# Optimization experiments

Measured on AMD Instinct MI355X. Metric: run time of the kernel, lower is better.

The kernel has to match this reference:

```python
import jax, jax.numpy as jnp
import numpy as np

TEMPERATURE = 0.1
BATCH_SIZE = 4096
NUM_CLASSES = 100
EPS = 1e-10
COS_EPS = 1e-8  # F.cosine_similarity default eps


def setup_inputs() -> dict:
    key = jax.random.key(0)
    k1, k2 = jax.random.split(key)
    pred = jax.random.normal(k1, (4096, 1024), dtype=jnp.float32)
    target = jax.random.randint(k2, (4096,), 0, NUM_CLASSES, dtype=jnp.int64)
    return {"pred": pred, "target": target}


def reference(pred, target):
    n, d = pred.shape
    # cosine similarity via normalize-once + Gram GEMM (same math as pairwise
    # F.cosine_similarity with its eps clamp on the norms)
    norms = jnp.linalg.norm(pred, axis=1, keepdims=True)  # [n,1]
    xn = pred / jnp.maximum(norms, COS_EPS)
    p_norm = xn @ xn.T                                    # [n,n]
    p_norm = jnp.maximum(p_norm, EPS)                     # p_norm[p_norm<eps]=eps
    dist = jnp.exp(p_norm / TEMPERATURE)

    same = target[:, None] == target[None, :]             # [n,n] bool
    eye = jnp.eye(n, dtype=dist.dtype)
    positives = same.astype(dist.dtype) - eye
    negatives = (~same).astype(dist.dtype)

    denominators = jnp.sum(dist * negatives, axis=0)      # [n]
    denominators = jnp.maximum(denominators, EPS)
    numerators = dist * positives
    frac = numerators / denominators[None, :]             # broadcast over rows

    # original does boolean indexing frac[frac>=eps]; equivalent masked log-sum
    valid = frac >= EPS
    safe = jnp.where(valid, frac, 1.0)
    loss = -jnp.sum(jnp.where(valid, jnp.log(safe), 0.0)) / BATCH_SIZE
    return loss
```

## Files before the change

kernel.cpp:

```cpp
#include <hip/hip_runtime.h>
#include <hip/hip_bf16.h>

#define NROWS 4096
#define DIM   1024
#define BT    256
#define BH    128
#define BK    128
#define NKT   (DIM / BK)
#define NTB   (NROWS / BT)
#define NOFF  240
#define TEMP_INV 10.0f
#define INV_S 3.814697e-6f

typedef int i32x4 __attribute__((ext_vector_type(4)));

__device__ __forceinline__ void gload16(const void* g, void* l) {
    __builtin_amdgcn_global_load_lds(
        (const __attribute__((address_space(1))) void*)g,
        (__attribute__((address_space(3))) void*)l, 16, 0, 0);
}

__global__ __launch_bounds__(256) void normalize_k(const float* __restrict__ pred,
                                                   unsigned char* __restrict__ xn,
                                                   float* __restrict__ posw,
                                                   float* __restrict__ denw) {
    const int row = blockIdx.x;
    const int tid = threadIdx.x;
    const float4 v = reinterpret_cast<const float4*>(pred + (size_t)row * DIM)[tid];
    float ss = v.x * v.x + v.y * v.y + v.z * v.z + v.w * v.w;
    #pragma unroll
    for (int off = 32; off; off >>= 1) ss += __shfl_xor(ss, off, 64);
    __shared__ float red[4];
    if ((tid & 63) == 0) red[tid >> 6] = ss;
    __syncthreads();
    const float tot = red[0] + red[1] + red[2] + red[3];
    const float scale = 512.0f / fmaxf(sqrtf(tot), 1e-8f);
    int q0 = __float2int_rn(v.x * scale);
    int q1 = __float2int_rn(v.y * scale);
    int q2 = __float2int_rn(v.z * scale);
    int q3 = __float2int_rn(v.w * scale);
    q0 = min(max(q0, -127), 127); q1 = min(max(q1, -127), 127);
    q2 = min(max(q2, -127), 127); q3 = min(max(q3, -127), 127);
    const int pk = (q0 & 0xFF) | ((q1 & 0xFF) << 8) |
                   ((q2 & 0xFF) << 16) | ((q3 & 0xFF) << 24);
    reinterpret_cast<int*>(xn)[row * (DIM / 4) + tid] = pk;
    if (tid == 0) { posw[row] = 0.0f; denw[row] = 0.0f; }
}

#define BAR asm volatile("s_barrier" ::: "memory")

__global__ __launch_bounds__(512, 2) void fused_gram(
        const unsigned char* __restrict__ xn, const int* __restrict__ tgt,
        float* __restrict__ posw, float* __restrict__ denw) {
    __shared__ unsigned char As[2][BT * BK];
    __shared__ unsigned char Bs[2][BH * BK];

    const int tid = threadIdx.x;
    const int w   = tid >> 6;
    const int l   = tid & 63;
    const int l15 = l & 15;
    const int kgl = l >> 4;
    const int swz = l15 & 7;

    int xr[2];
    #pragma unroll
    for (int s = 0; s < 2; ++s) xr[s] = ((s * 4 + kgl) ^ swz) * 16;

    if ((int)blockIdx.x < NOFF) {
        const int t = ((int)blockIdx.x & 7) * (NOFF / 8) + ((int)blockIdx.x >> 3);
        const int tau = t >> 1, half = t & 1;
        int bi = 0, rem = tau;
        while (rem >= NTB - 1 - bi) { rem -= NTB - 1 - bi; ++bi; }
        const int bj = bi + 1 + rem;
        const int rowbase = bi * BT;
        const int colbase = bj * BT + half * BH;

        const int wm = w >> 1;
        const int wn = w & 1;

        const unsigned char* arow = xn + (size_t)rowbase * DIM;
        const unsigned char* bcol = xn + (size_t)colbase * DIM;

        int rowA[4], rowB[4];
        #pragma unroll
        for (int fi = 0; fi < 4; ++fi) rowA[fi] = (wm * 64 + fi * 16 + l15) * BK;
        #pragma unroll
        for (int fj = 0; fj < 4; ++fj) rowB[fj] = (wn * 64 + fj * 16 + l15) * BK;

        i32x4 acc[4][4];
        #pragma unroll
        for (int i = 0; i < 4; ++i)
            #pragma unroll
            for (int j = 0; j < 4; ++j) acc[i][j] = (i32x4){0, 0, 0, 0};

#define STAGE_OD(kt_, s_)                                                      \
    do {                                                                       \
        _Pragma("unroll")                                                      \
        for (int c = 0; c < 4; ++c) {                                          \
            const int p = c * 512 + tid, r = p >> 3, kg = (p & 7) ^ (r & 7);   \
            gload16(arow + (size_t)r * DIM + (kt_) * BK + kg * 16,             \
                    &As[s_][p * 16]);                                          \
        }                                                                      \
        _Pragma("unroll")                                                      \
        for (int c = 0; c < 2; ++c) {                                          \
            const int p = c * 512 + tid, r = p >> 3, kg = (p & 7) ^ (r & 7);   \
            gload16(bcol + (size_t)r * DIM + (kt_) * BK + kg * 16,             \
                    &Bs[s_][p * 16]);                                          \
        }                                                                      \
    } while (0)

        STAGE_OD(0, 0);
        for (int kt = 0; kt < NKT; ++kt) {
            const int cur = kt & 1;
            if (kt + 1 < NKT) {
                STAGE_OD(kt + 1, cur ^ 1);
                asm volatile("s_waitcnt vmcnt(6)" ::: "memory");
            } else {
                asm volatile("s_waitcnt vmcnt(0)" ::: "memory");
            }
            BAR;
            const unsigned char* as = &As[cur][0];
            const unsigned char* bs = &Bs[cur][0];
            #pragma unroll
            for (int s = 0; s < 2; ++s) {
                i32x4 a[4], b[4];
                #pragma unroll
                for (int fi = 0; fi < 4; ++fi)
                    a[fi] = *reinterpret_cast<const i32x4*>(&as[rowA[fi] + xr[s]]);
                #pragma unroll
                for (int fj = 0; fj < 4; ++fj)
                    b[fj] = *reinterpret_cast<const i32x4*>(&bs[rowB[fj] + xr[s]]);
                __builtin_amdgcn_s_setprio(1);
                #pragma unroll
                for (int fi = 0; fi < 4; ++fi)
                    #pragma unroll
                    for (int fj = 0; fj < 4; ++fj)
                        acc[fi][fj] = __builtin_amdgcn_mfma_i32_16x16x64_i8(
                            a[fi], b[fj], acc[fi][fj], 0, 0, 0);
                __builtin_amdgcn_s_setprio(0);
            }
            BAR;
        }
#undef STAGE_OD

        int jc[4], tj[4];
        #pragma unroll
        for (int fj = 0; fj < 4; ++fj) {
            jc[fj] = colbase + wn * 64 + fj * 16 + l15;
            tj[fj] = tgt[jc[fj]];
        }
        float denc[4] = {0.f, 0.f, 0.f, 0.f};
        float posc[4] = {0.f, 0.f, 0.f, 0.f};
        #pragma unroll
        for (int fi = 0; fi < 4; ++fi) {
            const int ribase = rowbase + wm * 64 + fi * 16 + (l >> 4) * 4;
            const int4 tiv = *reinterpret_cast<const int4*>(&tgt[ribase]);
            const int tia[4] = {tiv.x, tiv.y, tiv.z, tiv.w};
            float denr[4] = {0.f, 0.f, 0.f, 0.f};
            float posr[4] = {0.f, 0.f, 0.f, 0.f};
            #pragma unroll
            for (int q = 0; q < 4; ++q) {
                const int ti = tia[q];
                #pragma unroll
                for (int fj = 0; fj < 4; ++fj) {
                    const float sv = (float)acc[fi][fj][q] * INV_S;
                    const float pc = fmaxf(sv, 1e-10f);
                    const float e  = __expf(TEMP_INV * pc);
                    if (ti != tj[fj]) { denc[fj] += e;  denr[q] += e; }
                    else              { posc[fj] += pc; posr[q] += pc; }
                }
            }
            #pragma unroll
            for (int q = 0; q < 4; ++q) {
                #pragma unroll
                for (int off = 1; off < 16; off <<= 1) {
                    denr[q] += __shfl_xor(denr[q], off, 64);
                    posr[q] += __shfl_xor(posr[q], off, 64);
                }
            }
            if (l15 == 0) {
                #pragma unroll
                for (int q = 0; q < 4; ++q) {
                    atomicAdd(&denw[ribase + q], denr[q]);
                    atomicAdd(&posw[ribase + q], posr[q]);
                }
            }
        }
        #pragma unroll
        for (int fj = 0; fj < 4; ++fj) {
            #pragma unroll
            for (int off = 16; off < 64; off <<= 1) {
                denc[fj] += __shfl_xor(denc[fj], off, 64);
                posc[fj] += __shfl_xor(posc[fj], off, 64);
            }
            if (l < 16) {
                atomicAdd(&denw[jc[fj]], denc[fj]);
                atomicAdd(&posw[jc[fj]], posc[fj]);
            }
        }
    } else {
        const int d = (int)blockIdx.x - NOFF;
        const int rowbase = d * BT;
        const int colbase = rowbase;
        const int wr = w >> 2;
        const int wc = w & 3;

        const unsigned char* arow = xn + (size_t)rowbase * DIM;

        int rowA[8], rowB[4];
        #pragma unroll
        for (int fi = 0; fi < 8; ++fi) rowA[fi] = (wr * 128 + fi * 16 + l15) * BK;
        #pragma unroll
        for (int fj = 0; fj < 4; ++fj) rowB[fj] = (wc * 64 + fj * 16 + l15) * BK;

        i32x4 acc[8][4];
        #pragma unroll
        for (int i = 0; i < 8; ++i)
            #pragma unroll
            for (int j = 0; j < 4; ++j) acc[i][j] = (i32x4){0, 0, 0, 0};

#define STAGE_DG(kt_, s_)                                                      \
    do {                                                                       \
        _Pragma("unroll")                                                      \
        for (int c = 0; c < 4; ++c) {                                          \
            const int p = c * 512 + tid, r = p >> 3, kg = (p & 7) ^ (r & 7);   \
            gload16(arow + (size_t)r * DIM + (kt_) * BK + kg * 16,             \
                    &As[s_][p * 16]);                                          \
        }                                                                      \
    } while (0)

        STAGE_DG(0, 0);
        for (int kt = 0; kt < NKT; ++kt) {
            const int cur = kt & 1;
            if (kt + 1 < NKT) {
                STAGE_DG(kt + 1, cur ^ 1);
                asm volatile("s_waitcnt vmcnt(4)" ::: "memory");
            } else {
                asm volatile("s_waitcnt vmcnt(0)" ::: "memory");
            }
            BAR;
            const unsigned char* as = &As[cur][0];
            #pragma unroll
            for (int s = 0; s < 2; ++s) {
                i32x4 a[8], b[4];
                #pragma unroll
                for (int fi = 0; fi < 8; ++fi)
                    a[fi] = *reinterpret_cast<const i32x4*>(&as[rowA[fi] + xr[s]]);
                #pragma unroll
                for (int fj = 0; fj < 4; ++fj)
                    b[fj] = *reinterpret_cast<const i32x4*>(&as[rowB[fj] + xr[s]]);
                __builtin_amdgcn_s_setprio(1);
                #pragma unroll
                for (int fi = 0; fi < 8; ++fi)
                    #pragma unroll
                    for (int fj = 0; fj < 4; ++fj)
                        acc[fi][fj] = __builtin_amdgcn_mfma_i32_16x16x64_i8(
                            a[fi], b[fj], acc[fi][fj], 0, 0, 0);
                __builtin_amdgcn_s_setprio(0);
            }
            BAR;
        }
#undef STAGE_DG

        int jc[4], tj[4];
        #pragma unroll
        for (int fj = 0; fj < 4; ++fj) {
            jc[fj] = colbase + wc * 64 + fj * 16 + l15;
            tj[fj] = tgt[jc[fj]];
        }
        float denc[4] = {0.f, 0.f, 0.f, 0.f};
        float posc[4] = {0.f, 0.f, 0.f, 0.f};
        #pragma unroll
        for (int fi = 0; fi < 8; ++fi) {
            const int ribase = rowbase + wr * 128 + fi * 16 + (l >> 4) * 4;
            const int4 tiv = *reinterpret_cast<const int4*>(&tgt[ribase]);
            const int tia[4] = {tiv.x, tiv.y, tiv.z, tiv.w};
            #pragma unroll
            for (int q = 0; q < 4; ++q) {
                const int gi = ribase + q;
                const int ti = tia[q];
                #pragma unroll
                for (int fj = 0; fj < 4; ++fj) {
                    const float sv = (float)acc[fi][fj][q] * INV_S;
                    const float pc = fmaxf(sv, 1e-10f);
                    const float e  = __expf(TEMP_INV * pc);
                    if (ti != tj[fj])        denc[fj] += e;
                    else if (gi != jc[fj])   posc[fj] += pc;
                }
            }
        }
        #pragma unroll
        for (int fj = 0; fj < 4; ++fj) {
            #pragma unroll
            for (int off = 16; off < 64; off <<= 1) {
                denc[fj] += __shfl_xor(denc[fj], off, 64);
                posc[fj] += __shfl_xor(posc[fj], off, 64);
            }
            if (l < 16) {
                atomicAdd(&denw[jc[fj]], denc[fj]);
                atomicAdd(&posw[jc[fj]], posc[fj]);
            }
        }
    }
}

__global__ __launch_bounds__(1024) void finalize_k(const float* __restrict__ posw,
                                                   const float* __restrict__ denw,
                                                   const int* __restrict__ tgt,
                                                   float* __restrict__ out) {
    __shared__ int hist[128];
    __shared__ float red[16];
    const int tid = threadIdx.x;
    if (tid < 128) hist[tid] = 0;
    __syncthreads();
    const int4 t4 = reinterpret_cast<const int4*>(tgt)[tid];
    atomicAdd(&hist[t4.x], 1);
    atomicAdd(&hist[t4.y], 1);
    atomicAdd(&hist[t4.z], 1);
    atomicAdd(&hist[t4.w], 1);
    __syncthreads();
    const int ta[4] = {t4.x, t4.y, t4.z, t4.w};
    float v = 0.0f;
    #pragma unroll
    for (int q = 0; q < 4; ++q) {
        const int j = tid * 4 + q;
        const float d = fmaxf(denw[j], 1e-10f);
        const float c = (float)(hist[ta[q]] - 1);
        v += TEMP_INV * posw[j] - c * __logf(d);
    }
    #pragma unroll
    for (int off = 32; off; off >>= 1) v += __shfl_xor(v, off, 64);
    if ((tid & 63) == 0) red[tid >> 6] = v;
    __syncthreads();
    if (tid == 0) {
        float s = 0.0f;
        #pragma unroll
        for (int i = 0; i < 16; ++i) s += red[i];
        out[0] = -s * (1.0f / 4096.0f);
    }
}

extern "C" void kernel_launch(void* const* d_in, const int* in_sizes, int n_in,
                              void* d_out, int out_size, void* d_ws, size_t ws_size,
                              hipStream_t stream) {
    const float* pred = (const float*)d_in[0];
    const int*   tgt  = (const int*)d_in[1];
    float* out = (float*)d_out;

    unsigned char* xn = (unsigned char*)d_ws;
    float* posw = (float*)((char*)d_ws + (size_t)NROWS * DIM);
    float* denw = posw + NROWS;

    normalize_k<<<NROWS, 256, 0, stream>>>(pred, xn, posw, denw);

    fused_gram<<<256, 512, 0, stream>>>(xn, tgt, posw, denw);

    finalize_k<<<1, 1024, 0, stream>>>(posw, denw, tgt, out);
}
```

Baseline: 34.34 us.

## Use FP4 scaled MFMA for off-diagonal Gram tiles, keep int8 for diagonal

The normalize kernel now writes a second copy of the normalized rows, quantized to FP4 (e2m1) with scale 32, next to the int8 copy. Off-diagonal Gram tiles read this half-size buffer and use the 16x16x128 f8f6f4 scaled MFMA with unit scales, which halves the K-loop iterations and the bytes staged through LDS. Diagonal tiles stay on the int8 path. The cost is much coarser quantization of the similarities that feed exp(10x), which risks loss accuracy, plus extra quantization work and workspace in the normalize step.

```diff
diff --git a/kernel.cpp b/kernel.cpp
--- a/kernel.cpp
+++ b/kernel.cpp
@@ -3,16 +3,23 @@
 
 #define NROWS 4096
 #define DIM   1024
+#define ROWB8 1024
+#define ROWB4 512
 #define BT    256
 #define BH    128
-#define BK    128
-#define NKT   (DIM / BK)
+#define BK8   128
+#define NKT8  (DIM / 128)
+#define BKB4  128
+#define NKT4  (DIM / 256)
 #define NTB   (NROWS / BT)
 #define NOFF  240
 #define TEMP_INV 10.0f
-#define INV_S 3.814697e-6f
+#define INV_S8 3.814697e-6f
+#define INV_S4 9.765625e-4f
+#define SCALE1 0x7F7F7F7F
 
 typedef int i32x4 __attribute__((ext_vector_type(4)));
+typedef int i32x8 __attribute__((ext_vector_type(8)));
 
 __device__ __forceinline__ void gload16(const void* g, void* l) {
     __builtin_amdgcn_global_load_lds(
@@ -20,8 +27,18 @@
         (__attribute__((address_space(3))) void*)l, 16, 0, 0);
 }
 
+__device__ __forceinline__ unsigned qfp4(float x) {
+    const float m = fabsf(x);
+    const unsigned c = (unsigned)(m >= 0.25f) + (unsigned)(m >= 0.75f)
+                     + (unsigned)(m >= 1.25f) + (unsigned)(m >= 1.75f)
+                     + (unsigned)(m >= 2.5f)  + (unsigned)(m >= 3.5f)
+                     + (unsigned)(m >= 5.0f);
+    return c | (x < 0.0f ? 8u : 0u);
+}
+
 __global__ __launch_bounds__(256) void normalize_k(const float* __restrict__ pred,
-                                                   unsigned char* __restrict__ xn,
+                                                   unsigned char* __restrict__ xn8,
+                                                   unsigned short* __restrict__ xn4,
                                                    float* __restrict__ posw,
                                                    float* __restrict__ denw) {
     const int row = blockIdx.x;
@@ -34,26 +51,31 @@
     if ((tid & 63) == 0) red[tid >> 6] = ss;
     __syncthreads();
     const float tot = red[0] + red[1] + red[2] + red[3];
-    const float scale = 512.0f / fmaxf(sqrtf(tot), 1e-8f);
-    int q0 = __float2int_rn(v.x * scale);
-    int q1 = __float2int_rn(v.y * scale);
-    int q2 = __float2int_rn(v.z * scale);
-    int q3 = __float2int_rn(v.w * scale);
+    const float inv = 1.0f / fmaxf(sqrtf(tot), 1e-8f);
+    const float s8 = 512.0f * inv;
+    int q0 = __float2int_rn(v.x * s8), q1 = __float2int_rn(v.y * s8);
+    int q2 = __float2int_rn(v.z * s8), q3 = __float2int_rn(v.w * s8);
     q0 = min(max(q0, -127), 127); q1 = min(max(q1, -127), 127);
     q2 = min(max(q2, -127), 127); q3 = min(max(q3, -127), 127);
-    const int pk = (q0 & 0xFF) | ((q1 & 0xFF) << 8) |
-                   ((q2 & 0xFF) << 16) | ((q3 & 0xFF) << 24);
-    reinterpret_cast<int*>(xn)[row * (DIM / 4) + tid] = pk;
+    reinterpret_cast<int*>(xn8)[row * (DIM / 4) + tid] =
+        (q0 & 0xFF) | ((q1 & 0xFF) << 8) | ((q2 & 0xFF) << 16) | ((q3 & 0xFF) << 24);
+    const float s4 = 32.0f * inv;
+    const unsigned f0 = qfp4(v.x * s4), f1 = qfp4(v.y * s4);
+    const unsigned f2 = qfp4(v.z * s4), f3 = qfp4(v.w * s4);
+    xn4[row * (ROWB4 / 2) + tid] =
+        (unsigned short)(f0 | (f1 << 4) | (f2 << 8) | (f3 << 12));
     if (tid == 0) { posw[row] = 0.0f; denw[row] = 0.0f; }
 }
 
 #define BAR asm volatile("s_barrier" ::: "memory")
 
 __global__ __launch_bounds__(512, 2) void fused_gram(
-        const unsigned char* __restrict__ xn, const int* __restrict__ tgt,
+        const unsigned char* __restrict__ xn8,
+        const unsigned char* __restrict__ xn4,
+        const int* __restrict__ tgt,
         float* __restrict__ posw, float* __restrict__ denw) {
-    __shared__ unsigned char As[2][BT * BK];
-    __shared__ unsigned char Bs[2][BH * BK];
+    __shared__ unsigned char As[2][BT * 128];
+    __shared__ unsigned char Bs[2][BH * 128];
 
     const int tid = threadIdx.x;
     const int w   = tid >> 6;
@@ -78,41 +100,41 @@
         const int wm = w >> 1;
         const int wn = w & 1;
 
-        const unsigned char* arow = xn + (size_t)rowbase * DIM;
-        const unsigned char* bcol = xn + (size_t)colbase * DIM;
+        const unsigned char* arow = xn4 + (size_t)rowbase * ROWB4;
+        const unsigned char* bcol = xn4 + (size_t)colbase * ROWB4;
 
         int rowA[4], rowB[4];
         #pragma unroll
-        for (int fi = 0; fi < 4; ++fi) rowA[fi] = (wm * 64 + fi * 16 + l15) * BK;
-        #pragma unroll
-        for (int fj = 0; fj < 4; ++fj) rowB[fj] = (wn * 64 + fj * 16 + l15) * BK;
-
-        i32x4 acc[4][4];
-        #pragma unroll
-        for (int i = 0; i < 4; ++i)
-            #pragma unroll
-            for (int j = 0; j < 4; ++j) acc[i][j] = (i32x4){0, 0, 0, 0};
+        for (int fi = 0; fi < 4; ++fi) rowA[fi] = (wm * 64 + fi * 16 + l15) * 128;
+        #pragma unroll
+        for (int fj = 0; fj < 4; ++fj) rowB[fj] = (wn * 64 + fj * 16 + l15) * 128;
+
+        float acc[4][4][4];
+        typedef float f32x4 __attribute__((ext_vector_type(4)));
+        f32x4* accv = reinterpret_cast<f32x4*>(acc);
+        #pragma unroll
+        for (int i = 0; i < 16; ++i) accv[i] = (f32x4){0.f, 0.f, 0.f, 0.f};
 
 #define STAGE_OD(kt_, s_)                                                      \
     do {                                                                       \
         _Pragma("unroll")                                                      \
         for (int c = 0; c < 4; ++c) {                                          \
             const int p = c * 512 + tid, r = p >> 3, kg = (p & 7) ^ (r & 7);   \
-            gload16(arow + (size_t)r * DIM + (kt_) * BK + kg * 16,             \
+            gload16(arow + (size_t)r * ROWB4 + (kt_) * BKB4 + kg * 16,         \
                     &As[s_][p * 16]);                                          \
         }                                                                      \
         _Pragma("unroll")                                                      \
         for (int c = 0; c < 2; ++c) {                                          \
             const int p = c * 512 + tid, r = p >> 3, kg = (p & 7) ^ (r & 7);   \
-            gload16(bcol + (size_t)r * DIM + (kt_) * BK + kg * 16,             \
+            gload16(bcol + (size_t)r * ROWB4 + (kt_) * BKB4 + kg * 16,         \
                     &Bs[s_][p * 16]);                                          \
         }                                                                      \
     } while (0)
 
         STAGE_OD(0, 0);
-        for (int kt = 0; kt < NKT; ++kt) {
+        for (int kt = 0; kt < NKT4; ++kt) {
             const int cur = kt & 1;
-            if (kt + 1 < NKT) {
+            if (kt + 1 < NKT4) {
                 STAGE_OD(kt + 1, cur ^ 1);
                 asm volatile("s_waitcnt vmcnt(6)" ::: "memory");
             } else {
@@ -122,22 +144,43 @@
             const unsigned char* as = &As[cur][0];
             const unsigned char* bs = &Bs[cur][0];
             #pragma unroll
-            for (int s = 0; s < 2; ++s) {
-                i32x4 a[4], b[4];
-                #pragma unroll
-                for (int fi = 0; fi < 4; ++fi)
-                    a[fi] = *reinterpret_cast<const i32x4*>(&as[rowA[fi] + xr[s]]);
-                #pragma unroll
-                for (int fj = 0; fj < 4; ++fj)
-                    b[fj] = *reinterpret_cast<const i32x4*>(&bs[rowB[fj] + xr[s]]);
-                __builtin_amdgcn_s_setprio(1);
-                #pragma unroll
-                for (int fi = 0; fi < 4; ++fi)
+            for (int m = 0; m < 2; ++m) {
+                #pragma unroll
+                for (int fjh = 0; fjh < 4; fjh += 2) {
+                    i32x8 b2[2];
                     #pragma unroll
-                    for (int fj = 0; fj < 4; ++fj)
-                        acc[fi][fj] = __builtin_amdgcn_mfma_i32_16x16x64_i8(
-                            a[fi], b[fj], acc[fi][fj], 0, 0, 0);
-                __builtin_amdgcn_s_setprio(0);
+                    for (int v2 = 0; v2 < 2; ++v2) {
+                        const i32x4 p = *reinterpret_cast<const i32x4*>(
+                            &bs[rowB[fjh + v2] + xr[m]]);
+                        i32x8 r; r[0]=p[0]; r[1]=p[1]; r[2]=p[2]; r[3]=p[3];
+                                 r[4]=p[0]; r[5]=p[1]; r[6]=p[2]; r[7]=p[3];
+                        b2[v2] = r;
+                    }
+                    #pragma unroll
+                    for (int fih = 0; fih < 4; fih += 2) {
+                        i32x8 a2[2];
+                        #pragma unroll
+                        for (int u = 0; u < 2; ++u) {
+                            const i32x4 p = *reinterpret_cast<const i32x4*>(
+                                &as[rowA[fih + u] + xr[m]]);
+                            i32x8 r; r[0]=p[0]; r[1]=p[1]; r[2]=p[2]; r[3]=p[3];
+                                     r[4]=p[0]; r[5]=p[1]; r[6]=p[2]; r[7]=p[3];
+                            a2[u] = r;
+                        }
+                        __builtin_amdgcn_s_setprio(1);
+                        #pragma unroll
+                        for (int u = 0; u < 2; ++u)
+                            #pragma unroll
+                            for (int v2 = 0; v2 < 2; ++v2) {
+                                f32x4* c = reinterpret_cast<f32x4*>(
+                                    acc[fih + u][fjh + v2]);
+                                *c = __builtin_amdgcn_mfma_scale_f32_16x16x128_f8f6f4(
+                                    a2[u], b2[v2], *c,
+                                    4, 4, 0, SCALE1, 0, SCALE1);
+                            }
+                        __builtin_amdgcn_s_setprio(0);
+                    }
+                }
             }
             BAR;
         }
@@ -163,7 +206,7 @@
                 const int ti = tia[q];
                 #pragma unroll
                 for (int fj = 0; fj < 4; ++fj) {
-                    const float sv = (float)acc[fi][fj][q] * INV_S;
+                    const float sv = acc[fi][fj][q] * INV_S4;
                     const float pc = fmaxf(sv, 1e-10f);
                     const float e  = __expf(TEMP_INV * pc);
                     if (ti != tj[fj]) { denc[fj] += e;  denr[q] += e; }
@@ -205,13 +248,13 @@
         const int wr = w >> 2;
         const int wc = w & 3;
 
-        const unsigned char* arow = xn + (size_t)rowbase * DIM;
+        const unsigned char* arow = xn8 + (size_t)rowbase * ROWB8;
 
         int rowA[8], rowB[4];
         #pragma unroll
-        for (int fi = 0; fi < 8; ++fi) rowA[fi] = (wr * 128 + fi * 16 + l15) * BK;
-        #pragma unroll
-        for (int fj = 0; fj < 4; ++fj) rowB[fj] = (wc * 64 + fj * 16 + l15) * BK;
+        for (int fi = 0; fi < 8; ++fi) rowA[fi] = (wr * 128 + fi * 16 + l15) * BK8;
+        #pragma unroll
+        for (int fj = 0; fj < 4; ++fj) rowB[fj] = (wc * 64 + fj * 16 + l15) * BK8;
 
         i32x4 acc[8][4];
         #pragma unroll
@@ -224,15 +267,15 @@
         _Pragma("unroll")                                                      \
         for (int c = 0; c < 4; ++c) {                                          \
             const int p = c * 512 + tid, r = p >> 3, kg = (p & 7) ^ (r & 7);   \
-            gload16(arow + (size_t)r * DIM + (kt_) * BK + kg * 16,             \
+            gload16(arow + (size_t)r * ROWB8 + (kt_) * BK8 + kg * 16,          \
                     &As[s_][p * 16]);                                          \
         }                                                                      \
     } while (0)
 
         STAGE_DG(0, 0);
-        for (int kt = 0; kt < NKT; ++kt) {
+        for (int kt = 0; kt < NKT8; ++kt) {
             const int cur = kt & 1;
-            if (kt + 1 < NKT) {
+            if (kt + 1 < NKT8) {
                 STAGE_DG(kt + 1, cur ^ 1);
                 asm volatile("s_waitcnt vmcnt(4)" ::: "memory");
             } else {
@@ -281,7 +324,7 @@
                 const int ti = tia[q];
                 #pragma unroll
                 for (int fj = 0; fj < 4; ++fj) {
-                    const float sv = (float)acc[fi][fj][q] * INV_S;
+                    const float sv = (float)acc[fi][fj][q] * INV_S8;
                     const float pc = fmaxf(sv, 1e-10f);
                     const float e  = __expf(TEMP_INV * pc);
                     if (ti != tj[fj])        denc[fj] += e;
@@ -347,13 +390,15 @@
     const int*   tgt  = (const int*)d_in[1];
     float* out = (float*)d_out;
 
-    unsigned char* xn = (unsigned char*)d_ws;
-    float* posw = (float*)((char*)d_ws + (size_t)NROWS * DIM);
+    unsigned char*  xn8 = (unsigned char*)d_ws;
+    unsigned short* xn4 = (unsigned short*)((char*)d_ws + (size_t)NROWS * ROWB8);
+    float* posw = (float*)((char*)d_ws + (size_t)NROWS * (ROWB8 + ROWB4));
     float* denw = posw + NROWS;
 
-    normalize_k<<<NROWS, 256, 0, stream>>>(pred, xn, posw, denw);
-
-    fused_gram<<<256, 512, 0, stream>>>(xn, tgt, posw, denw);
+    normalize_k<<<NROWS, 256, 0, stream>>>(pred, xn8, xn4, posw, denw);
+
+    fused_gram<<<256, 512, 0, stream>>>(xn8, (const unsigned char*)xn4,
+                                        tgt, posw, denw);
 
     finalize_k<<<1, 1024, 0, stream>>>(posw, denw, tgt, out);
 }
```

Measured after the change: 54.16 us. +57.7%, slower.
